# Optimization experiments

Measured on AMD Instinct MI355X. Metric: run time of the kernel, lower is better.

The kernel has to match this reference:

```python
import jax, jax.numpy as jnp
import numpy as np

N = 100000          # num nodes
E = 1600000         # num edges (before self loops)
IN_C = 128
OUT_C = 64
RATIO = 0.5
NEG_SLOPE = 0.2


def setup_inputs() -> dict:
    key = jax.random.key(0)
    k1, k2, k3, k4, k5 = jax.random.split(key, 5)
    x = jax.random.normal(k1, (N, IN_C), jnp.float32)
    # edges with no self loops (module removes then re-adds self loops)
    src = jax.random.randint(k2, (E,), 0, N, dtype=jnp.int32)
    off = jax.random.randint(k3, (E,), 1, N, dtype=jnp.int32)
    tgt = (src + off) % N
    edge_index = jnp.stack([src, tgt])  # [2, E], row0=source(j), row1=target(i)
    # glorot init
    s_w = float(np.sqrt(6.0 / (IN_C + OUT_C)))
    weight = jax.random.uniform(k4, (IN_C, OUT_C), jnp.float32, -s_w, s_w)
    s_a = float(np.sqrt(6.0 / (1 + 2 * OUT_C)))
    att = jax.random.uniform(k5, (1, 2 * OUT_C), jnp.float32, -s_a, s_a)
    batch = jnp.zeros((N,), jnp.int32)  # single graph
    return {"x": x, "weight": weight, "att": att,
            "edge_index": edge_index, "batch": batch, "bn": 0}


def reference(x, weight, att, edge_index, batch, bn):
    # add self loops (static shapes: E + N edges)
    loops = jnp.arange(N, dtype=edge_index.dtype)
    src = jnp.concatenate([edge_index[0], loops])  # edge_index_j (source)
    tgt = jnp.concatenate([edge_index[1], loops])  # edge_index_i (target)

    h = x @ weight                      # [N, OUT_C]
    x_j = h[src]                        # [E+N, OUT_C] gathered source feats
    x_i = h[tgt]

    # alpha = (cat([x_i, x_j]) * att).sum(-1)
    alpha = x_i @ att[0, :OUT_C] + x_j @ att[0, OUT_C:]   # [E+N]
    alpha = jnp.where(alpha > 0, alpha, NEG_SLOPE * alpha)  # leaky_relu

    # edge-softmax grouped by target node (every node has a self loop -> no empty segment)
    m = jax.ops.segment_max(alpha, tgt, num_segments=N)
    a = jnp.exp(alpha - m[tgt])
    denom = jax.ops.segment_sum(a, tgt, num_segments=N)
    alpha = a / (denom[tgt] + 1e-16)

    # node importance = sum of attention over outgoing edges (grouped by source)
    alpha_sum = jax.ops.segment_sum(alpha, src, num_segments=N)

    # topk node selection (ratio of all nodes; single graph)
    k = int(np.ceil(RATIO * N))
    _, topk_idx = jax.lax.top_k(alpha_sum, k)
    node_mask = jnp.zeros((N,), bool).at[topk_idx].set(True)

    # filter_dn: keep edges whose both endpoints survive; mask instead of compacting
    edge_mask = node_mask[src] & node_mask[tgt]
    alpha_m = jnp.where(edge_mask, alpha, 0.0)

    # weighted scatter-add aggregation to target nodes (aggr='add')
    out = jax.ops.segment_sum(alpha_m[:, None] * x_j, tgt, num_segments=N)  # [N, OUT_C]
    # bn flag is 0 -> BatchNorm skipped
    return out, edge_mask, node_mask
```

## Files before the change

### kernel.cpp

```cpp
#include <hip/hip_runtime.h>
#include <stdint.h>

#define IN_C 128
#define OUT_C 64
#define NEG_SLOPE 0.2f
#define RB 256
#define RBINS 512
#define STAGE 8192
#define NGH (RBINS * RB)
#define NGHS (RBINS * RBINS)
#define KC 8
#define SXW 192

typedef unsigned int u32;
typedef unsigned long long u64;

__device__ __forceinline__ u32 fenc(float f) {
  u32 u = __float_as_uint(f);
  return (u & 0x80000000u) ? ~u : (u | 0x80000000u);
}
__device__ __forceinline__ u64 key64(float v, int i) {
  return (((u64)fenc(v)) << 32) | (u64)(0xffffffffu - (u32)i);
}

__global__ __launch_bounds__(128) void k_gemm(const float* __restrict__ x,
                                              const float* __restrict__ w,
                                              const float* __restrict__ att,
                                              float* __restrict__ h,
                                              float* __restrict__ ai, float* __restrict__ aj,
                                              int N) {
  __shared__ float sw[IN_C * OUT_C];
  __shared__ float sx[KC * SXW];
  int tid = threadIdx.x;
  int rbase = blockIdx.x * 128;

  for (int i = tid; i < (IN_C * OUT_C) / 4; i += 128)
    ((float4*)sw)[i] = ((const float4*)w)[i];

  int c0 = (tid & 7) * 8;
  int rg = tid >> 3;
  int sxbase = rg * 12;
  float acc[8][8];
#pragma unroll
  for (int i = 0; i < 8; i++)
#pragma unroll
    for (int j = 0; j < 8; j++) acc[i][j] = 0.f;

  int grow = rbase + tid;
  int base = (tid >> 3) * 12 + (tid & 7);
  const float* xp = &x[(size_t)grow * IN_C];

  float4 pv0 = make_float4(0.f, 0.f, 0.f, 0.f);
  float4 pv1 = make_float4(0.f, 0.f, 0.f, 0.f);
  if (grow < N) {
    pv0 = *(const float4*)&xp[0];
    pv1 = *(const float4*)&xp[4];
  }

  for (int kb = 0; kb < IN_C; kb += KC) {
    __syncthreads();
    sx[0 * SXW + base] = pv0.x;
    sx[1 * SXW + base] = pv0.y;
    sx[2 * SXW + base] = pv0.z;
    sx[3 * SXW + base] = pv0.w;
    sx[4 * SXW + base] = pv1.x;
    sx[5 * SXW + base] = pv1.y;
    sx[6 * SXW + base] = pv1.z;
    sx[7 * SXW + base] = pv1.w;
    if (kb + KC < IN_C && grow < N) {
      pv0 = *(const float4*)&xp[kb + KC];
      pv1 = *(const float4*)&xp[kb + KC + 4];
    }
    __syncthreads();
#pragma unroll
    for (int kl = 0; kl < KC; ++kl) {
      int kg = kb + kl;
      float xr[8], wv[8];
      *(float4*)&xr[0] = *(const float4*)&sx[kl * SXW + sxbase];
      *(float4*)&xr[4] = *(const float4*)&sx[kl * SXW + sxbase + 4];
      *(float4*)&wv[0] = *(const float4*)&sw[kg * OUT_C + c0];
      *(float4*)&wv[4] = *(const float4*)&sw[kg * OUT_C + c0 + 4];
#pragma unroll
      for (int i = 0; i < 8; ++i)
#pragma unroll
        for (int j = 0; j < 8; ++j)
          acc[i][j] += xr[i] * wv[j];
    }
  }

  float pi[8], pj[8];
#pragma unroll
  for (int i = 0; i < 8; ++i) { pi[i] = 0.f; pj[i] = 0.f; }
#pragma unroll
  for (int j = 0; j < 8; ++j) {
    float a0 = att[c0 + j], a1 = att[OUT_C + c0 + j];
#pragma unroll
    for (int i = 0; i < 8; ++i) {
      pi[i] += acc[i][j] * a0;
      pj[i] += acc[i][j] * a1;
    }
  }
#pragma unroll
  for (int o = 1; o < 8; o <<= 1) {
#pragma unroll
    for (int i = 0; i < 8; ++i) {
      pi[i] += __shfl_xor(pi[i], o);
      pj[i] += __shfl_xor(pj[i], o);
    }
  }
#pragma unroll
  for (int i = 0; i < 8; ++i) {
    int row = rbase + rg * 8 + i;
    if (row < N) {
      *(float4*)&h[(size_t)row * OUT_C + c0]     = make_float4(acc[i][0], acc[i][1], acc[i][2], acc[i][3]);
      *(float4*)&h[(size_t)row * OUT_C + c0 + 4] = make_float4(acc[i][4], acc[i][5], acc[i][6], acc[i][7]);
      if ((tid & 7) == 0) { ai[row] = pi[i]; aj[row] = pj[i]; }
    }
  }
}

__global__ __launch_bounds__(256) void k_rhist_t(const int* __restrict__ tgt,
                                                 int E, int EN, int chunk, u32* __restrict__ gh,
                                                 u32* __restrict__ hist8, u32* __restrict__ done,
                                                 u32* __restrict__ sel, u32* __restrict__ cnt, u32 k) {
  __shared__ u32 lh[RBINS];
  int tid = threadIdx.x, b = blockIdx.x;
  if (b == 0) {
    for (int i = tid; i < 2048; i += 256) hist8[i] = 0u;
    if (tid < 8) { done[tid] = 0u; cnt[tid] = 0u; }
    if (tid == 0) { sel[0] = 0u; sel[1] = 0u; sel[2] = k; sel[3] = 0u; }
  }
  for (int d = tid; d < RBINS; d += 256) lh[d] = 0u;
  __syncthreads();
  int lo = b * chunk, hi = min(lo + chunk, EN);
  for (int e = lo + tid; e < hi; e += 256) {
    int t = (e < E) ? tgt[e] : e - E;
    atomicAdd(&lh[((u32)t) >> 8], 1u);
  }
  __syncthreads();
  for (int d = tid; d < RBINS; d += 256) gh[d * RB + b] = lh[d];
}

__global__ __launch_bounds__(256) void k_scanA(const u32* __restrict__ in, u32* __restrict__ out,
                                               u32* __restrict__ bsum, int n) {
  __shared__ u32 s[256];
  int i = blockIdx.x * 256 + threadIdx.x;
  u32 v = (i < n) ? in[i] : 0u;
  s[threadIdx.x] = v;
  __syncthreads();
  for (int o = 1; o < 256; o <<= 1) {
    u32 t = (threadIdx.x >= (unsigned)o) ? s[threadIdx.x - o] : 0u;
    __syncthreads();
    s[threadIdx.x] += t;
    __syncthreads();
  }
  if (i < n) out[i] = s[threadIdx.x] - v;
  if (threadIdx.x == 255) bsum[blockIdx.x] = s[255];
}

__global__ __launch_bounds__(1024) void k_scanB(u32* __restrict__ bsum, int nb) {
  __shared__ u32 s[1024];
  int tid = threadIdx.x;
  u32 v = (tid < nb) ? bsum[tid] : 0u;
  s[tid] = v;
  __syncthreads();
  for (int o = 1; o < 1024; o <<= 1) {
    u32 t = (tid >= o) ? s[tid - o] : 0u;
    __syncthreads();
    s[tid] += t;
    __syncthreads();
  }
  if (tid < nb) bsum[tid] = s[tid] - v;
}

__global__ __launch_bounds__(256) void k_scanC(u32* __restrict__ out, const u32* __restrict__ bsum, int n) {
  int i = blockIdx.x * 256 + threadIdx.x;
  if (i < n) out[i] += bsum[blockIdx.x];
}

__global__ __launch_bounds__(256) void k_rscatter_t(const int* __restrict__ src, const int* __restrict__ tgt,
                                                    int E, int EN, int chunk,
                                                    const u32* __restrict__ gh, u32* __restrict__ bufB) {
  __shared__ u32 cnt[RBINS];
  int tid = threadIdx.x, b = blockIdx.x;
  for (int d = tid; d < RBINS; d += 256) cnt[d] = gh[d * RB + b];
  __syncthreads();
  int lo = b * chunk, hi = min(lo + chunk, EN);
  for (int e = lo + tid; e < hi; e += 256) {
    int s, t;
    if (e < E) { s = src[e]; t = tgt[e]; } else { s = t = e - E; }
    u32 p = atomicAdd(&cnt[((u32)t) >> 8], 1u);
    bufB[p] = (((u32)t & 255u) << 24) | (u32)s;
  }
}

__global__ __launch_bounds__(256) void k_rpass2(const u32* __restrict__ in, u32* __restrict__ out,
                                                const u32* __restrict__ gh, u32* __restrict__ ghs,
                                                u32* __restrict__ offT,
                                                const float* __restrict__ ai, const float* __restrict__ aj,
                                                float* __restrict__ alpha,
                                                int N, int EN) {
  __shared__ u32 hist[256];
  __shared__ u32 sc[256];
  __shared__ u32 lhs[RBINS];
  __shared__ u32 stage[STAGE];
  int tid = threadIdx.x, d = blockIdx.x;
  u32 start = gh[d * RB];
  u32 end = (d < RBINS - 1) ? gh[(d + 1) * RB] : (u32)EN;
  int sz = (int)(end - start);
  hist[tid] = 0u;
  for (int dd = tid; dd < RBINS; dd += 256) lhs[dd] = 0u;
  __syncthreads();
  for (u32 p = start + tid; p < end; p += 256) {
    u32 it = in[p];
    atomicAdd(&hist[it >> 24], 1u);
    atomicAdd(&lhs[(it & 0xffffffu) >> 8], 1u);
  }
  __syncthreads();
  for (int dd = tid; dd < RBINS; dd += 256) ghs[dd * RBINS + d] = lhs[dd];
  u32 hv = hist[tid];
  sc[tid] = hv;
  __syncthreads();
  for (int o = 1; o < 256; o <<= 1) {
    u32 t = (tid >= o) ? sc[tid - o] : 0u;
    __syncthreads();
    sc[tid] += t;
    __syncthreads();
  }
  u32 excl = sc[tid] - hv;
  int node = (d << 8) + tid;
  if (node < N) offT[node] = start + excl;
  if (node == 0) offT[N] = (u32)EN;
  hist[tid] = excl;
  __syncthreads();
  bool staged = (sz <= STAGE);
  for (u32 p = start + tid; p < end; p += 256) {
    u32 it = in[p];
    u32 lp = atomicAdd(&hist[it >> 24], 1u);
    if (staged) stage[lp] = it;
    else out[start + lp] = it;
  }
  __syncthreads();
  if (staged)
    for (int i = tid; i < sz; i += 256) out[start + i] = stage[i];
  __syncthreads();
  if (node < N) {
    int lb = (tid > 0) ? (int)sc[tid - 1] : 0;
    int le = (int)sc[tid];
    float an = ai[node];
    float mx = -1e30f;
    for (int i = lb; i < le; ++i) {
      u32 it = staged ? stage[i] : out[start + i];
      float a = an + aj[it & 0xffffffu];
      a = a > 0.f ? a : NEG_SLOPE * a;
      mx = fmaxf(mx, a);
      if (staged) stage[i] = __float_as_uint(a);
    }
    float sm = 0.f;
    for (int i = lb; i < le; ++i) {
      float a;
      if (staged) a = __uint_as_float(stage[i]);
      else {
        u32 it = out[start + i];
        a = an + aj[it & 0xffffffu];
        a = a > 0.f ? a : NEG_SLOPE * a;
      }
      float v = expf(a - mx);
      sm += v;
      if (staged) stage[i] = __float_as_uint(v);
      else alpha[start + i] = v;
    }
    float inv = 1.f / (sm + 1e-16f);
    for (int i = lb; i < le; ++i) {
      float v = staged ? __uint_as_float(stage[i]) : alpha[start + i];
      alpha[start + i] = v * inv;
    }
  }
}

__global__ __launch_bounds__(256) void k_rscatter_s(const u32* __restrict__ csr,
                                                    const float* __restrict__ alpha,
                                                    const u32* __restrict__ gh, const u32* __restrict__ ghs,
                                                    u64* __restrict__ bufB, int EN) {
  __shared__ u32 cnt[RBINS];
  int tid = threadIdx.x, d = blockIdx.x;
  for (int dd = tid; dd < RBINS; dd += 256) cnt[dd] = ghs[dd * RBINS + d];
  __syncthreads();
  u32 start = gh[d * RB];
  u32 end = (d < RBINS - 1) ? gh[(d + 1) * RB] : (u32)EN;
  for (u32 e = start + tid; e < end; e += 256) {
    u32 s = csr[e] & 0xffffffu;
    u32 p = atomicAdd(&cnt[s >> 8], 1u);
    bufB[p] = (((u64)(s & 255u)) << 32) | __float_as_uint(alpha[e]);
  }
}

__global__ __launch_bounds__(256) void k_asum_acc(const u64* __restrict__ bufB,
                                                  const u32* __restrict__ ghs,
                                                  float* __restrict__ asum,
                                                  u32* __restrict__ hist8, u32* __restrict__ done,
                                                  u32* __restrict__ sel,
                                                  int N, int EN, int nblk) {
  __shared__ float sums[256];
  __shared__ u32 lh[256];
  __shared__ u32 s[256];
  __shared__ u32 sres;
  int tid = threadIdx.x, d = blockIdx.x;
  u32 start = ghs[d * RBINS];
  u32 end = (d < RBINS - 1) ? ghs[(d + 1) * RBINS] : (u32)EN;
  sums[tid] = 0.f;
  __syncthreads();
  for (u32 p = start + tid; p < end; p += 256) {
    u64 it = bufB[p];
    atomicAdd(&sums[(u32)(it >> 32)], __uint_as_float((u32)it));
  }
  __syncthreads();
  int node = d * 256 + tid;
  u32 bin = 256u;
  if (node < N) {
    float v = sums[tid];
    asum[node] = v;
    bin = (u32)(key64(v, node) >> 56) & 255u;
  }
  lh[tid] = 0u;
  __syncthreads();
  if (bin < 256u) atomicAdd(&lh[bin], 1u);
  __syncthreads();
  if (lh[tid]) atomicAdd(&hist8[tid], lh[tid]);
  __syncthreads();
  if (tid == 0)
    sres = __hip_atomic_fetch_add(&done[0], 1u, __ATOMIC_ACQ_REL, __HIP_MEMORY_SCOPE_AGENT);
  __syncthreads();
  if (sres == (u32)(nblk - 1)) {
    u32 krem = sel[2];
    u32 hv = __hip_atomic_load(&hist8[255 - tid], __ATOMIC_RELAXED, __HIP_MEMORY_SCOPE_AGENT);
    s[tid] = hv;
    __syncthreads();
    for (int o = 1; o < 256; o <<= 1) {
      u32 t = (tid >= o) ? s[tid - o] : 0u;
      __syncthreads();
      s[tid] += t;
      __syncthreads();
    }
    u32 cum = s[tid], prev = (tid > 0) ? s[tid - 1] : 0u;
    if (cum >= krem && prev < krem) {
      int dsel = 255 - tid;
      ((u64*)sel)[0] = (u64)(u32)dsel;
      sel[2] = krem - prev;
    }
  }
}

__global__ __launch_bounds__(256) void k_histpick(const float* __restrict__ asum,
                                                  const u32* __restrict__ list_in, const u32* __restrict__ cnt_in,
                                                  u32* __restrict__ list_out, u32* __restrict__ cnt_out,
                                                  u32* __restrict__ hist8, u32* __restrict__ done,
                                                  u32* __restrict__ sel, int N, int pass, int nblk) {
  __shared__ u32 lh[256];
  __shared__ u32 sres;
  __shared__ u32 s[256];
  int tid = threadIdx.x;
  lh[tid] = 0u;
  __syncthreads();
  u64 prefix = ((const u64*)sel)[0];
  int shift = 56 - 8 * pass;
  int n = list_in ? (int)*cnt_in : N;
  int i = blockIdx.x * 256 + tid;
  if (i < n) {
    int idx = list_in ? (int)list_in[i] : i;
    u64 k = key64(asum[idx], idx);
    bool ok = (pass == 0) || ((k >> (shift + 8)) == prefix);
    if (ok) {
      atomicAdd(&lh[(u32)(k >> shift) & 255u], 1u);
      if (list_out) {
        u32 p = atomicAdd(cnt_out, 1u);
        list_out[p] = (u32)idx;
      }
    }
  }
  __syncthreads();
  if (lh[tid]) atomicAdd(&hist8[pass * 256 + tid], lh[tid]);
  __syncthreads();
  if (tid == 0)
    sres = __hip_atomic_fetch_add(&done[pass], 1u, __ATOMIC_ACQ_REL, __HIP_MEMORY_SCOPE_AGENT);
  __syncthreads();
  if (sres == (u32)(nblk - 1)) {
    u32 krem = sel[2];
    u32 hv = __hip_atomic_load(&hist8[pass * 256 + (255 - tid)], __ATOMIC_RELAXED,
                               __HIP_MEMORY_SCOPE_AGENT);
    s[tid] = hv;
    __syncthreads();
    for (int o = 1; o < 256; o <<= 1) {
      u32 t = (tid >= o) ? s[tid - o] : 0u;
      __syncthreads();
      s[tid] += t;
      __syncthreads();
    }
    u32 cum = s[tid], prev = (tid > 0) ? s[tid - 1] : 0u;
    if (cum >= krem && prev < krem) {
      int dsel = 255 - tid;
      ((u64*)sel)[0] = (prefix << 8) | (u64)(u32)dsel;
      sel[2] = krem - prev;
    }
  }
}

__global__ __launch_bounds__(256) void k_finish(const float* __restrict__ asum,
                                                const u32* __restrict__ list, const u32* __restrict__ cntp,
                                                u32* __restrict__ sel) {
  __shared__ u64 keys[2048];
  __shared__ u32 cc;
  int tid = threadIdx.x;
  if (tid == 0) cc = 0u;
  __syncthreads();
  int n = (int)*cntp;
  u32 fsel = (u32)((const u64*)sel)[0];
  u32 krem = sel[2];
  for (int i = tid; i < n; i += 256) {
    int idx = (int)list[i];
    u64 k = key64(asum[idx], idx);
    if ((u32)(k >> 32) == fsel) {
      u32 p = atomicAdd(&cc, 1u);
      if (p < 2048) keys[p] = k;
    }
  }
  __syncthreads();
  int C = (int)min(cc, 2048u);
  for (int i = tid; i < C; i += 256) {
    u64 k = keys[i];
    u32 rank = 0;
    for (int j = 0; j < C; ++j)
      if (keys[j] > k) rank++;
    if (rank == krem - 1) ((u64*)sel)[0] = k;
  }
}

__global__ __launch_bounds__(256) void k_node_mask(const float* __restrict__ asum,
                                                   const u32* __restrict__ sel,
                                                   u32* __restrict__ nm,
                                                   float* __restrict__ out_node, int N) {
  int i = blockIdx.x * 256 + threadIdx.x;
  if (i >= N) return;
  u64 T = ((const u64*)sel)[0];
  bool m = key64(asum[i], i) >= T;
  nm[i] = m ? 1u : 0u;
  out_node[i] = m ? 1.f : 0.f;
}

__global__ __launch_bounds__(256) void k_mask(const int* __restrict__ src, const int* __restrict__ tgt,
                                              const u32* __restrict__ nm,
                                              float* __restrict__ out_edge,
                                              int E, int EN) {
  int e = blockIdx.x * 256 + threadIdx.x;
  if (e >= EN) return;
  int s, t;
  if (e < E) { s = src[e]; t = tgt[e]; } else { s = t = e - E; }
  out_edge[e] = (nm[s] && nm[t]) ? 1.f : 0.f;
}

__global__ __launch_bounds__(256) void k_aggregate(const u32* __restrict__ off,
                                                   const u32* __restrict__ csr,
                                                   const float* __restrict__ alpha,
                                                   const float* __restrict__ h,
                                                   const u32* __restrict__ nm,
                                                   float* __restrict__ out, int N) {
  int node = blockIdx.x * 4 + (threadIdx.x >> 6);
  int lane = threadIdx.x & 63;
  int g = lane >> 4;
  int c = lane & 15;
  if (node >= N) return;
  float4 acc = make_float4(0.f, 0.f, 0.f, 0.f);
  if (nm[node]) {
    u32 b = off[node], e2 = off[node + 1];
    for (u32 p0 = b; p0 < e2; p0 += 16) {
      float av[4];
      u32 sv[4];
#pragma unroll
      for (int q = 0; q < 4; ++q) {
        u32 p = p0 + q * 4 + (u32)g;
        bool ok = p < e2;
        u32 pp = ok ? p : b;
        u32 sp = csr[pp] & 0xffffffu;
        float a = alpha[pp];
        sv[q] = sp;
        av[q] = (ok && nm[sp]) ? a : 0.f;
      }
      float4 hv[4];
#pragma unroll
      for (int q = 0; q < 4; ++q) {
        hv[q] = make_float4(0.f, 0.f, 0.f, 0.f);
        if (av[q] != 0.f)
          hv[q] = *(const float4*)&h[(size_t)sv[q] * OUT_C + c * 4];
      }
#pragma unroll
      for (int q = 0; q < 4; ++q) {
        acc.x += av[q] * hv[q].x;
        acc.y += av[q] * hv[q].y;
        acc.z += av[q] * hv[q].z;
        acc.w += av[q] * hv[q].w;
      }
    }
#pragma unroll
    for (int o = 16; o < 64; o <<= 1) {
      acc.x += __shfl_xor(acc.x, o);
      acc.y += __shfl_xor(acc.y, o);
      acc.z += __shfl_xor(acc.z, o);
      acc.w += __shfl_xor(acc.w, o);
    }
  }
  if (g == 0)
    *(float4*)&out[(size_t)node * OUT_C + c * 4] = acc;
}

extern "C" void kernel_launch(void* const* d_in, const int* in_sizes, int n_in,
                              void* d_out, int out_size, void* d_ws, size_t ws_size,
                              hipStream_t stream) {
  const float* x   = (const float*)d_in[0];
  const float* w   = (const float*)d_in[1];
  const float* att = (const float*)d_in[2];
  const int*   ei  = (const int*)d_in[3];

  int N = in_sizes[0] / IN_C;
  int E = in_sizes[3] / 2;
  int EN = E + N;
  const int* src = ei;
  const int* tgt = ei + E;

  float* out      = (float*)d_out;
  float* out_edge = out + (size_t)N * OUT_C;
  float* out_node = out_edge + (size_t)EN;

  char* p = (char*)d_ws;
  auto alloc = [&](size_t bytes) -> char* {
    char* r = p;
    p += (bytes + 255) & ~(size_t)255;
    return r;
  };
  float* h     = (float*)alloc((size_t)N * OUT_C * 4);
  float* ai    = (float*)alloc((size_t)N * 4);
  float* aj    = (float*)alloc((size_t)N * 4);
  u32*   bufA  = (u32*)alloc((size_t)EN * 4);
  u64*   bufB  = (u64*)alloc((size_t)EN * 8);
  float* alpha = (float*)alloc((size_t)EN * 4);
  u32*   offT  = (u32*)alloc((size_t)(N + 1) * 4);
  u32*   gh    = (u32*)alloc((size_t)NGH * 4);
  u32*   ghs   = (u32*)alloc((size_t)NGHS * 4);
  u32*   bsum  = (u32*)alloc(2048 * 4);
  float* asum  = (float*)alloc((size_t)N * 4);
  u32*   nm    = (u32*)alloc((size_t)N * 4);
  u32*   hist8 = (u32*)alloc(2048 * 4);
  u32*   done  = (u32*)alloc(8 * 4);
  u32*   cnt   = (u32*)alloc(8 * 4);
  u32*   sel   = (u32*)alloc(256);
  u32*   listA = (u32*)alloc((size_t)N * 4);
  u32*   listB = (u32*)alloc((size_t)N * 4);

  u32 kSel = (u32)((N + 1) / 2);
  int chunk = (EN + RB - 1) / RB;
  int nScanT = (NGH + 255) / 256;
  int nScanS = (NGHS + 255) / 256;
  int gGemm = (N + 127) / 128;
  int gN = (N + 255) / 256;
  int gE = (EN + 255) / 256;
  int gNode4 = (N + 3) / 4;

  k_gemm<<<gGemm, 128, 0, stream>>>(x, w, att, h, ai, aj, N);

  k_rhist_t<<<RB, 256, 0, stream>>>(tgt, E, EN, chunk, gh, hist8, done, sel, cnt, kSel);
  k_scanA<<<nScanT, 256, 0, stream>>>(gh, gh, bsum, NGH);
  k_scanB<<<1, 1024, 0, stream>>>(bsum, nScanT);
  k_scanC<<<nScanT, 256, 0, stream>>>(gh, bsum, NGH);
  k_rscatter_t<<<RB, 256, 0, stream>>>(src, tgt, E, EN, chunk, gh, (u32*)bufB);
  k_rpass2<<<RBINS, 256, 0, stream>>>((u32*)bufB, bufA, gh, ghs, offT, ai, aj, alpha, N, EN);

  k_scanA<<<nScanS, 256, 0, stream>>>(ghs, ghs, bsum, NGHS);
  k_scanB<<<1, 1024, 0, stream>>>(bsum, nScanS);
  k_scanC<<<nScanS, 256, 0, stream>>>(ghs, bsum, NGHS);
  k_rscatter_s<<<RBINS, 256, 0, stream>>>(bufA, alpha, gh, ghs, bufB, EN);
  k_asum_acc<<<RBINS, 256, 0, stream>>>(bufB, ghs, asum, hist8, done, sel, N, EN, RBINS);

  k_histpick<<<gN, 256, 0, stream>>>(asum, nullptr, nullptr, listA, &cnt[1],
                                     hist8, done, sel, N, 1, gN);
  k_histpick<<<gN, 256, 0, stream>>>(asum, listA, &cnt[1], listB, &cnt[2],
                                     hist8, done, sel, N, 2, gN);
  k_histpick<<<gN, 256, 0, stream>>>(asum, listB, &cnt[2], listA, &cnt[3],
                                     hist8, done, sel, N, 3, gN);
  k_finish<<<1, 256, 0, stream>>>(asum, listA, &cnt[3], sel);

  k_node_mask<<<gN, 256, 0, stream>>>(asum, sel, nm, out_node, N);
  k_mask<<<gE, 256, 0, stream>>>(src, tgt, nm, out_edge, E, EN);
  k_aggregate<<<gNode4, 256, 0, stream>>>(offT, bufA, alpha, h, nm, out, N);
}
```

Before: 362.4 us.

## Split GEMM K across two half-blocks and pre-pack masked edge pairs for aggregation

Result: no change. 368.3 us (+1.6%).

```diff
diff --git a/kernel.cpp b/kernel.cpp
--- a/kernel.cpp
+++ b/kernel.cpp
@@ -23,32 +23,35 @@
   return (((u64)fenc(v)) << 32) | (u64)(0xffffffffu - (u32)i);
 }
 
-__global__ __launch_bounds__(128) void k_gemm(const float* __restrict__ x,
+__global__ __launch_bounds__(256) void k_gemm(const float* __restrict__ x,
                                               const float* __restrict__ w,
                                               const float* __restrict__ att,
                                               float* __restrict__ h,
                                               float* __restrict__ ai, float* __restrict__ aj,
                                               int N) {
   __shared__ float sw[IN_C * OUT_C];
-  __shared__ float sx[KC * SXW];
+  __shared__ float sx[2][KC * SXW];
   int tid = threadIdx.x;
+  int half = tid >> 7;
+  int htid = tid & 127;
   int rbase = blockIdx.x * 128;
 
-  for (int i = tid; i < (IN_C * OUT_C) / 4; i += 128)
+  for (int i = tid; i < (IN_C * OUT_C) / 4; i += 256)
     ((float4*)sw)[i] = ((const float4*)w)[i];
 
-  int c0 = (tid & 7) * 8;
-  int rg = tid >> 3;
+  int c0 = (htid & 7) * 8;
+  int rg = htid >> 3;
   int sxbase = rg * 12;
+  float* sxh = sx[half];
   float acc[8][8];
 #pragma unroll
   for (int i = 0; i < 8; i++)
 #pragma unroll
     for (int j = 0; j < 8; j++) acc[i][j] = 0.f;
 
-  int grow = rbase + tid;
-  int base = (tid >> 3) * 12 + (tid & 7);
-  const float* xp = &x[(size_t)grow * IN_C];
+  int grow = rbase + htid;
+  int base = (htid >> 3) * 12 + (htid & 7);
+  const float* xp = &x[(size_t)grow * IN_C + half * 64];
 
   float4 pv0 = make_float4(0.f, 0.f, 0.f, 0.f);
   float4 pv1 = make_float4(0.f, 0.f, 0.f, 0.f);
@@ -57,27 +60,27 @@
     pv1 = *(const float4*)&xp[4];
   }
 
-  for (int kb = 0; kb < IN_C; kb += KC) {
-    __syncthreads();
-    sx[0 * SXW + base] = pv0.x;
-    sx[1 * SXW + base] = pv0.y;
-    sx[2 * SXW + base] = pv0.z;
-    sx[3 * SXW + base] = pv0.w;
-    sx[4 * SXW + base] = pv1.x;
-    sx[5 * SXW + base] = pv1.y;
-    sx[6 * SXW + base] = pv1.z;
-    sx[7 * SXW + base] = pv1.w;
-    if (kb + KC < IN_C && grow < N) {
+  for (int kb = 0; kb < 64; kb += KC) {
+    __syncthreads();
+    sxh[0 * SXW + base] = pv0.x;
+    sxh[1 * SXW + base] = pv0.y;
+    sxh[2 * SXW + base] = pv0.z;
+    sxh[3 * SXW + base] = pv0.w;
+    sxh[4 * SXW + base] = pv1.x;
+    sxh[5 * SXW + base] = pv1.y;
+    sxh[6 * SXW + base] = pv1.z;
+    sxh[7 * SXW + base] = pv1.w;
+    if (kb + KC < 64 && grow < N) {
       pv0 = *(const float4*)&xp[kb + KC];
       pv1 = *(const float4*)&xp[kb + KC + 4];
     }
     __syncthreads();
 #pragma unroll
     for (int kl = 0; kl < KC; ++kl) {
-      int kg = kb + kl;
+      int kg = half * 64 + kb + kl;
       float xr[8], wv[8];
-      *(float4*)&xr[0] = *(const float4*)&sx[kl * SXW + sxbase];
-      *(float4*)&xr[4] = *(const float4*)&sx[kl * SXW + sxbase + 4];
+      *(float4*)&xr[0] = *(const float4*)&sxh[kl * SXW + sxbase];
+      *(float4*)&xr[4] = *(const float4*)&sxh[kl * SXW + sxbase + 4];
       *(float4*)&wv[0] = *(const float4*)&sw[kg * OUT_C + c0];
       *(float4*)&wv[4] = *(const float4*)&sw[kg * OUT_C + c0 + 4];
 #pragma unroll
@@ -88,33 +91,52 @@
     }
   }
 
-  float pi[8], pj[8];
-#pragma unroll
-  for (int i = 0; i < 8; ++i) { pi[i] = 0.f; pj[i] = 0.f; }
-#pragma unroll
-  for (int j = 0; j < 8; ++j) {
-    float a0 = att[c0 + j], a1 = att[OUT_C + c0 + j];
+  __syncthreads();
+  if (half == 1) {
 #pragma unroll
     for (int i = 0; i < 8; ++i) {
-      pi[i] += acc[i][j] * a0;
-      pj[i] += acc[i][j] * a1;
-    }
-  }
-#pragma unroll
-  for (int o = 1; o < 8; o <<= 1) {
+      *(float4*)&sw[htid * 64 + i * 8]     = make_float4(acc[i][0], acc[i][1], acc[i][2], acc[i][3]);
+      *(float4*)&sw[htid * 64 + i * 8 + 4] = make_float4(acc[i][4], acc[i][5], acc[i][6], acc[i][7]);
+    }
+  }
+  __syncthreads();
+  if (half == 0) {
 #pragma unroll
     for (int i = 0; i < 8; ++i) {
-      pi[i] += __shfl_xor(pi[i], o);
-      pj[i] += __shfl_xor(pj[i], o);
-    }
-  }
-#pragma unroll
-  for (int i = 0; i < 8; ++i) {
-    int row = rbase + rg * 8 + i;
-    if (row < N) {
-      *(float4*)&h[(size_t)row * OUT_C + c0]     = make_float4(acc[i][0], acc[i][1], acc[i][2], acc[i][3]);
-      *(float4*)&h[(size_t)row * OUT_C + c0 + 4] = make_float4(acc[i][4], acc[i][5], acc[i][6], acc[i][7]);
-      if ((tid & 7) == 0) { ai[row] = pi[i]; aj[row] = pj[i]; }
+      float4 a0 = *(const float4*)&sw[htid * 64 + i * 8];
+      float4 a1 = *(const float4*)&sw[htid * 64 + i * 8 + 4];
+      acc[i][0] += a0.x; acc[i][1] += a0.y; acc[i][2] += a0.z; acc[i][3] += a0.w;
+      acc[i][4] += a1.x; acc[i][5] += a1.y; acc[i][6] += a1.z; acc[i][7] += a1.w;
+    }
+
+    float pi[8], pj[8];
+#pragma unroll
+    for (int i = 0; i < 8; ++i) { pi[i] = 0.f; pj[i] = 0.f; }
+#pragma unroll
+    for (int j = 0; j < 8; ++j) {
+      float a0 = att[c0 + j], a1 = att[OUT_C + c0 + j];
+#pragma unroll
+      for (int i = 0; i < 8; ++i) {
+        pi[i] += acc[i][j] * a0;
+        pj[i] += acc[i][j] * a1;
+      }
+    }
+#pragma unroll
+    for (int o = 1; o < 8; o <<= 1) {
+#pragma unroll
+      for (int i = 0; i < 8; ++i) {
+        pi[i] += __shfl_xor(pi[i], o);
+        pj[i] += __shfl_xor(pj[i], o);
+      }
+    }
+#pragma unroll
+    for (int i = 0; i < 8; ++i) {
+      int row = rbase + rg * 8 + i;
+      if (row < N) {
+        *(float4*)&h[(size_t)row * OUT_C + c0]     = make_float4(acc[i][0], acc[i][1], acc[i][2], acc[i][3]);
+        *(float4*)&h[(size_t)row * OUT_C + c0 + 4] = make_float4(acc[i][4], acc[i][5], acc[i][6], acc[i][7]);
+        if ((htid & 7) == 0) { ai[row] = pi[i]; aj[row] = pj[i]; }
+      }
     }
   }
 }
@@ -449,18 +471,21 @@
 
 __global__ __launch_bounds__(256) void k_mask(const int* __restrict__ src, const int* __restrict__ tgt,
                                               const u32* __restrict__ nm,
-                                              float* __restrict__ out_edge,
+                                              const u32* __restrict__ csr, const float* __restrict__ alpha,
+                                              float* __restrict__ out_edge, u64* __restrict__ pair,
                                               int E, int EN) {
   int e = blockIdx.x * 256 + threadIdx.x;
   if (e >= EN) return;
   int s, t;
   if (e < E) { s = src[e]; t = tgt[e]; } else { s = t = e - E; }
   out_edge[e] = (nm[s] && nm[t]) ? 1.f : 0.f;
+  u32 sp = csr[e] & 0xffffffu;
+  u32 ab = nm[sp] ? __float_as_uint(alpha[e]) : 0u;
+  pair[e] = (((u64)sp) << 32) | ab;
 }
 
 __global__ __launch_bounds__(256) void k_aggregate(const u32* __restrict__ off,
-                                                   const u32* __restrict__ csr,
-                                                   const float* __restrict__ alpha,
+                                                   const u64* __restrict__ pair,
                                                    const float* __restrict__ h,
                                                    const u32* __restrict__ nm,
                                                    float* __restrict__ out, int N) {
@@ -472,28 +497,27 @@
   float4 acc = make_float4(0.f, 0.f, 0.f, 0.f);
   if (nm[node]) {
     u32 b = off[node], e2 = off[node + 1];
-    for (u32 p0 = b; p0 < e2; p0 += 16) {
-      float av[4];
-      u32 sv[4];
-#pragma unroll
-      for (int q = 0; q < 4; ++q) {
+    for (u32 p0 = b; p0 < e2; p0 += 32) {
+      u64 pr[8];
+      float av[8];
+      u32 sv[8];
+#pragma unroll
+      for (int q = 0; q < 8; ++q) {
         u32 p = p0 + q * 4 + (u32)g;
         bool ok = p < e2;
-        u32 pp = ok ? p : b;
-        u32 sp = csr[pp] & 0xffffffu;
-        float a = alpha[pp];
-        sv[q] = sp;
-        av[q] = (ok && nm[sp]) ? a : 0.f;
-      }
-      float4 hv[4];
-#pragma unroll
-      for (int q = 0; q < 4; ++q) {
+        pr[q] = pair[ok ? p : b];
+        av[q] = ok ? __uint_as_float((u32)pr[q]) : 0.f;
+        sv[q] = (u32)(pr[q] >> 32);
+      }
+      float4 hv[8];
+#pragma unroll
+      for (int q = 0; q < 8; ++q) {
         hv[q] = make_float4(0.f, 0.f, 0.f, 0.f);
         if (av[q] != 0.f)
           hv[q] = *(const float4*)&h[(size_t)sv[q] * OUT_C + c * 4];
       }
 #pragma unroll
-      for (int q = 0; q < 4; ++q) {
+      for (int q = 0; q < 8; ++q) {
         acc.x += av[q] * hv[q].x;
         acc.y += av[q] * hv[q].y;
         acc.z += av[q] * hv[q].z;
@@ -564,7 +588,7 @@
   int gE = (EN + 255) / 256;
   int gNode4 = (N + 3) / 4;
 
-  k_gemm<<<gGemm, 128, 0, stream>>>(x, w, att, h, ai, aj, N);
+  k_gemm<<<gGemm, 256, 0, stream>>>(x, w, att, h, ai, aj, N);
 
   k_rhist_t<<<RB, 256, 0, stream>>>(tgt, E, EN, chunk, gh, hist8, done, sel, cnt, kSel);
   k_scanA<<<nScanT, 256, 0, stream>>>(gh, gh, bsum, NGH);
@@ -588,6 +612,6 @@
   k_finish<<<1, 256, 0, stream>>>(asum, listA, &cnt[3], sel);
 
   k_node_mask<<<gN, 256, 0, stream>>>(asum, sel, nm, out_node, N);
-  k_mask<<<gE, 256, 0, stream>>>(src, tgt, nm, out_edge, E, EN);
-  k_aggregate<<<gNode4, 256, 0, stream>>>(offT, bufA, alpha, h, nm, out, N);
-}
+  k_mask<<<gE, 256, 0, stream>>>(src, tgt, nm, bufA, alpha, out_edge, bufB, E, EN);
+  k_aggregate<<<gNode4, 256, 0, stream>>>(offT, bufB, h, nm, out, N);
+}
```
